# Kernel optimization log

Measured on AMD Instinct MI355X. Metric: run time of the kernel, lower is better.

The kernel has to match this reference:

```python
import jax, jax.numpy as jnp
import numpy as np

B, R, C, H, W = 8, 4, 64, 128, 128
RF, E = 256, 8
C2 = 2 * C
K = 3


def setup_inputs() -> dict:
    key = jax.random.key(0)
    ks = jax.random.split(key, 8)
    return {
        "x": jax.random.normal(ks[0], (B, C, H, W), jnp.float32),
        "routing": jax.random.normal(ks[1], (B, R, RF), jnp.float32),
        # nn.Linear(routing_features, num_experts)
        "routing_W": jax.random.normal(ks[2], (RF, E), jnp.float32) * 0.05,
        "routing_b": jnp.zeros((E,), jnp.float32),
        # CondConv2d expert weights: (E, Cout, Cin, k, k)
        "W1": jax.random.normal(ks[3], (E, C2, C, K, K), jnp.float32) * 0.04,
        "prelu_a": jnp.float32(0.25),  # PReLU single shared parameter
        "W2": jax.random.normal(ks[4], (E, C, C2, K, K), jnp.float32) * 0.03,
        # self-routing Linear(2*in_features, num_experts)
        "sr_W": jax.random.normal(ks[5], (C2, E), jnp.float32) * 0.08,
        "sr_b": jnp.zeros((E,), jnp.float32),
        # conv_output: Conv2d(in_features, 1, kernel_size=1) with bias
        "Wout": jax.random.normal(ks[6], (1, C), jnp.float32) * 0.1,
        "bout": jnp.zeros((1,), jnp.float32),
    }


def _prelu(x, a):
    return jnp.where(x >= 0, x, a * x)


def _cond_conv(x, rw, Wexp):
    # x: (B,Cin,H,W); rw: (B,E); Wexp: (E,Cout,Cin,k,k)
    # per-sample mixed kernel, then per-sample conv (vmap over batch)
    w = jnp.einsum('be,eoikl->boikl', rw, Wexp)
    def one(xi, wi):
        return jax.lax.conv_general_dilated(
            xi[None], wi, window_strides=(1, 1), padding=[(1, 1), (1, 1)])[0]
    return jax.vmap(one)(x, w)


def reference(x, routing, routing_W, routing_b, W1, prelu_a, W2, sr_W, sr_b, Wout, bout):
    rw = jax.nn.sigmoid(routing @ routing_W + routing_b)  # (B,R,E)
    rw = jnp.transpose(rw, (1, 0, 2))                     # (R,B,E)

    def per_head(rw_r):
        xc = _prelu(_cond_conv(x, rw_r, W1), prelu_a)      # (B,C2,H,W)
        pooled = xc.mean(axis=(2, 3))                      # adaptive_avg_pool2d(.,1)
        srw = pooled @ sr_W + sr_b                         # no sigmoid (per source)
        xc2 = _prelu(_cond_conv(xc, srw, W2), prelu_a)     # (B,C,H,W)
        out = jnp.einsum('bchw,oc->bohw', xc2, Wout)       # 1x1 conv
        return out + bout[None, :, None, None]             # (B,1,H,W)

    res = jax.vmap(per_head)(rw)                           # (R,B,1,H,W)
    return jnp.transpose(res[:, :, 0], (1, 0, 2, 3))       # (B,R,H,W)
```

## Files before the change

### kernel.cpp

```cpp
#include <hip/hip_runtime.h>
#include <stdint.h>


typedef _Float16 f16_t;
typedef _Float16 f16x8 __attribute__((ext_vector_type(8)));
typedef _Float16 f16x4 __attribute__((ext_vector_type(4)));
typedef float    f32x4 __attribute__((ext_vector_type(4)));

#define B_   8
#define R_   4
#define C_   64
#define C2_  128
#define H_   128
#define W_   128
#define E_   8
#define RF_  256
#define WP_  130
#define HP_  130

__device__ __forceinline__ f32x4 mfma16(f16x8 a, f16x8 b, f32x4 c) {
  return __builtin_amdgcn_mfma_f32_16x16x32_f16(a, b, c, 0, 0, 0);
}

__device__ __forceinline__ void gl16(const f16_t* g, f16_t* l) {
  __builtin_amdgcn_global_load_lds(
      (const __attribute__((address_space(1))) unsigned int*)(const void*)g,
      (__attribute__((address_space(3))) unsigned int*)(void*)l, 16, 0, 0);
}

__device__ __host__ __forceinline__ int sig(int n) { return (n ^ (n >> 2)) & 3; }

__global__ void k_rw(const float* __restrict__ routing, const float* __restrict__ rW,
                     const float* __restrict__ rB, float* __restrict__ rw,
                     float* __restrict__ pooled4) {
  int t = threadIdx.x;
  #pragma unroll
  for (int i = 0; i < 16; ++i) pooled4[i*256 + t] = 0.f;
  int e = t & 7, b = (t >> 3) & 7, r = t >> 6;
  float acc = rB[e];
  for (int f = 0; f < RF_; ++f)
    acc += routing[(b*R_ + r)*RF_ + f] * rW[f*E_ + e];
  rw[(r*B_ + b)*E_ + e] = 1.0f / (1.0f + __expf(-acc));
}

__global__ void k_zero(f16_t* __restrict__ xbt, f16_t* __restrict__ xct,
                       size_t xct_stride) {
  const f16x8 z = {0,0,0,0,0,0,0,0};
  int t = blockIdx.x*256 + threadIdx.x;
  if (t < 16640) {
    int ch = t & 7, u = t >> 3;
    int pix = u % 130; u /= 130;
    int rs = u & 1, b = u >> 1;
    *(f16x8*)&xbt[((size_t)(b*HP_ + rs*129)*WP_ + pix)*C_ + ch*8] = z;
    return;
  }
  t -= 16640;
  if (t < 133120) {
    int ch = t & 15, u = t >> 4;
    int pix = u % 130; u /= 130;
    int rs = u & 1; u >>= 1;
    int b = u & 7, r = u >> 3;
    *(f16x8*)&xct[(size_t)r*xct_stride + ((size_t)(b*HP_ + rs*129)*WP_ + pix)*C2_ + ch*8] = z;
    return;
  }
  t -= 133120;
  if (t < 131072) {
    int ch = t & 15, u = t >> 4;
    int hp = (u & 127) + 1; u >>= 7;
    int cs = u & 1; u >>= 1;
    int b = u & 7, r = u >> 3;
    *(f16x8*)&xct[(size_t)r*xct_stride + ((size_t)(b*HP_ + hp)*WP_ + cs*129)*C2_ + ch*8] = z;
  }
}

__global__ void k_xt(const float* __restrict__ x, f16_t* __restrict__ xbt) {
  int wh = blockIdx.x, h = blockIdx.y, b = blockIdx.z;
  int t = threadIdx.x;
  int w0 = wh * 64;
  __shared__ float tile[64][65];
  #pragma unroll
  for (int rep = 0; rep < 16; ++rep) {
    int idx = rep*256 + t;
    int c = idx >> 6, w = idx & 63;
    tile[c][w] = x[((size_t)(b*C_ + c)*H_ + h)*W_ + w0 + w];
  }
  __syncthreads();
  #pragma unroll
  for (int rep = 0; rep < 16; ++rep) {
    int idx = rep*256 + t;
    int w = idx >> 6, c = idx & 63;
    xbt[((size_t)(b*HP_ + h + 1)*WP_ + (w0 + w + 1))*C_ + c] = (f16_t)tile[c][w];
  }
  if (t < 64) {
    if (wh == 0) xbt[((size_t)(b*HP_ + h + 1)*WP_ + 0)*C_ + t]   = (f16_t)0.0f;
    else         xbt[((size_t)(b*HP_ + h + 1)*WP_ + 129)*C_ + t] = (f16_t)0.0f;
  }
}

__global__ void k_mix1(const float* __restrict__ rw, const float* __restrict__ W1,
                       f16_t* __restrict__ w1m) {
  int gid = blockIdx.x*256 + threadIdx.x;
  int cq4 = gid & 15;
  int s   = (gid >> 4) % 9;
  int t2  = (gid >> 4) / 9;
  int co  = t2 & 127;
  int rb  = t2 >> 7;
  float o0=0.f,o1=0.f,o2=0.f,o3=0.f;
  #pragma unroll
  for (int e = 0; e < E_; ++e) {
    float rv = rw[rb*E_ + e];
    const float* wp = W1 + (size_t)((e*C2_ + co)*C_ + cq4*4)*9 + s;
    o0 += rv*wp[0]; o1 += rv*wp[9]; o2 += rv*wp[18]; o3 += rv*wp[27];
  }
  f16x4 pk; pk[0]=(f16_t)o0; pk[1]=(f16_t)o1; pk[2]=(f16_t)o2; pk[3]=(f16_t)o3;
  int cb  = cq4 >> 3;
  int q   = (cq4 >> 1) & 3;
  int off = (cq4 & 1) * 4;
  size_t row = ((size_t)(rb*2 + cb)*128 + co);
  *(f16x4*)&w1m[row*288 + (size_t)(s*4 + (q ^ sig(co)))*8 + off] = pk;
}

__global__ void k_mix2(const float* __restrict__ pooled, const float* __restrict__ srW,
                       const float* __restrict__ srb, const float* __restrict__ W2,
                       f16_t* __restrict__ w2m, size_t w2m_stride, int r0) {
  const int r = r0 + blockIdx.y;
  const float* pooled_r = pooled + (size_t)r*B_*C2_;
  f16_t* w2m_r = w2m + (size_t)r*w2m_stride;
  __shared__ float sw[64];
  int t = threadIdx.x;
  if (t < 64) {
    int b = t >> 3, e = t & 7;
    float acc = srb[e];
    for (int c = 0; c < C2_; ++c)
      acc += pooled_r[b*C2_ + c] * (1.0f/16384.0f) * srW[c*E_ + e];
    sw[t] = acc;
  }
  __syncthreads();
  int gid = blockIdx.x*256 + t;
  int c2q = gid & 31;
  int s   = (gid >> 5) % 9;
  int t2  = (gid >> 5) / 9;
  int co  = t2 & 63;
  int b   = t2 >> 6;
  float o0=0.f,o1=0.f,o2=0.f,o3=0.f;
  #pragma unroll
  for (int e = 0; e < E_; ++e) {
    float rv = sw[b*E_ + e];
    const float* wp = W2 + (size_t)((e*C_ + co)*C2_ + c2q*4)*9 + s;
    o0 += rv*wp[0]; o1 += rv*wp[9]; o2 += rv*wp[18]; o3 += rv*wp[27];
  }
  f16x4 pk; pk[0]=(f16_t)o0; pk[1]=(f16_t)o1; pk[2]=(f16_t)o2; pk[3]=(f16_t)o3;
  int it  = c2q >> 3;
  int q   = (c2q >> 1) & 3;
  int off = (c2q & 1) * 4;
  size_t row = ((size_t)b*4 + it)*64 + co;
  *(f16x4*)&w2m_r[row*288 + (size_t)(s*4 + (q ^ sig(co)))*8 + off] = pk;
}

__global__ __launch_bounds__(512, 2) void k_conv1(
    const f16_t* __restrict__ xbt, const f16_t* __restrict__ w1m,
    const float* __restrict__ pa, f16_t* __restrict__ xct, size_t xct_stride,
    float* __restrict__ pooled, int r0)
{
  const int bx = blockIdx.x;
  const int b = bx & 7, h0 = (bx >> 3) << 2;
  const int r = r0 + blockIdx.z;
  f16_t* xct_r = xct + (size_t)blockIdx.z*xct_stride;
  float* pooled_r = pooled + (size_t)r*B_*C2_;
  const int tid = threadIdx.x;
  const int lane = tid & 63;
  const int wid = tid >> 6;
  const int wrow = wid >> 1, wm = wid & 1;
  const int l15 = lane & 15, l4 = lane >> 4;
  __shared__ __align__(16) f16_t lA[128*288];
  __shared__ __align__(16) f16_t lB[3120*8];

  const int xorA = (l4 ^ sig(l15)) << 4;
  int xorB[3];
  #pragma unroll
  for (int dw = 0; dw < 3; ++dw) xorB[dw] = (l4 ^ sig(l15 + dw)) << 4;

  f32x4 acc[4][8];
  #pragma unroll
  for (int i=0;i<4;++i)
    #pragma unroll
    for (int j=0;j<8;++j) acc[i][j] = (f32x4){0.f,0.f,0.f,0.f};

  const int rb = r*B_ + b;
  const f16_t* w1base = w1m + (size_t)rb*2*128*288;
  const f16_t* xb = xbt + ((size_t)(b*HP_ + h0))*WP_*C_;

  for (int cb = 0; cb < 2; ++cb) {
    __syncthreads();
    #pragma unroll
    for (int k = 0; k < 9; ++k) {
      int u = k*512 + tid;
      gl16(w1base + (size_t)cb*128*288 + (size_t)u*8, &lA[u*8]);
    }
    #pragma unroll
    for (int k = 0; k < 6; ++k) {
      int u = k*512 + tid;
      int lr = u / 520, rem = u - lr*520;
      int pix = rem >> 2, cq = (rem & 3) ^ sig(pix);
      gl16(xb + ((size_t)lr*WP_ + pix)*C_ + cb*32 + cq*8, &lB[u*8]);
    }
    if (tid < 48) {
      int u = 3072 + tid;
      int rem = u - 2600;
      int pix = rem >> 2, cq = (rem & 3) ^ sig(pix);
      gl16(xb + ((size_t)5*WP_ + pix)*C_ + cb*32 + cq*8, &lB[u*8]);
    }
    __syncthreads();
    __builtin_amdgcn_s_setprio(1);
    #pragma unroll
    for (int s = 0; s < 9; ++s) {
      const int dh = s / 3, dw = s % 3;
      f16x8 af[4];
      #pragma unroll
      for (int fm = 0; fm < 4; ++fm)
        af[fm] = *(const f16x8*)((const char*)lA
                   + (wm*64 + fm*16 + l15)*576 + s*64 + xorA);
      const char* bbase = (const char*)lB + (wrow + dh)*8320 + (l15 + dw)*64 + xorB[dw];
      f16x8 bf[8];
      #pragma unroll
      for (int fn = 0; fn < 8; ++fn)
        bf[fn] = *(const f16x8*)(bbase + fn*1024);
      #pragma unroll
      for (int fm = 0; fm < 4; ++fm)
        #pragma unroll
        for (int fn = 0; fn < 8; ++fn)
          acc[fm][fn] = mfma16(af[fm], bf[fn], acc[fm][fn]);
    }
    __builtin_amdgcn_s_setprio(0);
  }

  const float a = pa[0];
  float ps[4][4];
  #pragma unroll
  for (int fm=0;fm<4;++fm)
    #pragma unroll
    for (int j=0;j<4;++j) ps[fm][j] = 0.f;
  #pragma unroll
  for (int fm = 0; fm < 4; ++fm)
    #pragma unroll
    for (int fn = 0; fn < 8; ++fn)
      #pragma unroll
      for (int j = 0; j < 4; ++j) {
        float v = acc[fm][fn][j];
        v = (v >= 0.f) ? v : a*v;
        acc[fm][fn][j] = v;
        ps[fm][j] += v;
      }
  #pragma unroll
  for (int fm = 0; fm < 4; ++fm)
    #pragma unroll
    for (int j = 0; j < 4; ++j) {
      float s = ps[fm][j];
      s += __shfl_xor(s, 1, 64);
      s += __shfl_xor(s, 2, 64);
      s += __shfl_xor(s, 4, 64);
      s += __shfl_xor(s, 8, 64);
      if (l15 == 0)
        atomicAdd(&pooled_r[b*C2_ + wm*64 + fm*16 + l4*4 + j], s);
    }
  #pragma unroll
  for (int t4 = 0; t4 < 4; ++t4) {
    __syncthreads();
    if (wrow == t4) {
      #pragma unroll
      for (int fm = 0; fm < 4; ++fm)
        #pragma unroll
        for (int fn = 0; fn < 8; ++fn) {
          f16x4 pk;
          #pragma unroll
          for (int j = 0; j < 4; ++j) pk[j] = (f16_t)acc[fm][fn][j];
          int pix = fn*16 + l15;
          *(f16x4*)((char*)lB + pix*336 + wm*160 + (fm*16 + l4*4)*2) = pk;
        }
    }
    __syncthreads();
    #pragma unroll
    for (int k = 0; k < 4; ++k) {
      int idx = tid + 512*k;
      int pix = idx >> 4, u = idx & 15;
      f16x8 v = *(const f16x8*)((const char*)lB + pix*336 + u*16 + ((u >= 8) ? 32 : 0));
      *(f16x8*)(xct_r + ((size_t)(b*HP_ + h0 + t4 + 1)*WP_ + pix + 1)*C2_ + u*8) = v;
    }
  }
}

__global__ __launch_bounds__(512, 2) void k_conv2(
    const f16_t* __restrict__ xct, size_t xct_stride,
    const f16_t* __restrict__ w2m, size_t w2m_stride,
    const float* __restrict__ pa, const float* __restrict__ Wout,
    const float* __restrict__ bout, float* __restrict__ out, int r0)
{
  const int bx = blockIdx.x;
  const int b = bx & 7, h0 = (bx >> 3) << 3;
  const int r = r0 + blockIdx.y;
  const int tid = threadIdx.x;
  const int lane = tid & 63;
  const int wid = tid >> 6;
  const int l15 = lane & 15, l4 = lane >> 4;
  __shared__ __align__(16) f16_t lA[64*288];
  __shared__ __align__(16) f16_t lB[5200*8];

  const int xorA = (l4 ^ sig(l15)) << 4;
  int xorB[3];
  #pragma unroll
  for (int dw = 0; dw < 3; ++dw) xorB[dw] = (l4 ^ sig(l15 + dw)) << 4;

  f32x4 acc[4][8];
  #pragma unroll
  for (int i=0;i<4;++i)
    #pragma unroll
    for (int j=0;j<8;++j) acc[i][j] = (f32x4){0.f,0.f,0.f,0.f};

  const f16_t* w2base = w2m + (size_t)r*w2m_stride + (size_t)b*4*64*288;
  const f16_t* xb = xct + (size_t)blockIdx.y*xct_stride + ((size_t)(b*HP_ + h0))*WP_*C2_;

  for (int it = 0; it < 4; ++it) {
    __syncthreads();
    #pragma unroll
    for (int k = 0; k < 4; ++k) {
      int u = k*512 + tid;
      gl16(w2base + (size_t)it*64*288 + (size_t)u*8, &lA[u*8]);
    }
    if (tid < 256) {
      int u = 2048 + tid;
      gl16(w2base + (size_t)it*64*288 + (size_t)u*8, &lA[u*8]);
    }
    #pragma unroll
    for (int k = 0; k < 10; ++k) {
      int u = k*512 + tid;
      int lr = u / 520, rem = u - lr*520;
      int pix = rem >> 2, cq = (rem & 3) ^ sig(pix);
      gl16(xb + ((size_t)lr*WP_ + pix)*C2_ + it*32 + cq*8, &lB[u*8]);
    }
    if (tid < 80) {
      int u = 5120 + tid;
      int rem = u - 4680;
      int pix = rem >> 2, cq = (rem & 3) ^ sig(pix);
      gl16(xb + ((size_t)9*WP_ + pix)*C2_ + it*32 + cq*8, &lB[u*8]);
    }
    __syncthreads();
    __builtin_amdgcn_s_setprio(1);
    #pragma unroll
    for (int s = 0; s < 9; ++s) {
      const int dh = s / 3, dw = s % 3;
      f16x8 af[4];
      #pragma unroll
      for (int fm = 0; fm < 4; ++fm)
        af[fm] = *(const f16x8*)((const char*)lA + (fm*16 + l15)*576 + s*64 + xorA);
      const char* bbase = (const char*)lB + (wid + dh)*8320 + (l15 + dw)*64 + xorB[dw];
      f16x8 bf[8];
      #pragma unroll
      for (int fn = 0; fn < 8; ++fn)
        bf[fn] = *(const f16x8*)(bbase + fn*1024);
      #pragma unroll
      for (int fm = 0; fm < 4; ++fm)
        #pragma unroll
        for (int fn = 0; fn < 8; ++fn)
          acc[fm][fn] = mfma16(af[fm], bf[fn], acc[fm][fn]);
    }
    __builtin_amdgcn_s_setprio(0);
  }

  const float a  = pa[0];
  const float bo = bout[0];
  float wr_[4][4];
  #pragma unroll
  for (int fm = 0; fm < 4; ++fm)
    #pragma unroll
    for (int j = 0; j < 4; ++j)
      wr_[fm][j] = Wout[fm*16 + l4*4 + j];
  float* orow = out + ((size_t)((b*R_ + r)*H_ + h0 + wid))*W_;
  #pragma unroll
  for (int fn = 0; fn < 8; ++fn) {
    float s = 0.f;
    #pragma unroll
    for (int fm = 0; fm < 4; ++fm)
      #pragma unroll
      for (int j = 0; j < 4; ++j) {
        float v = acc[fm][fn][j];
        v = (v >= 0.f) ? v : a*v;
        s += wr_[fm][j]*v;
      }
    s += __shfl_xor(s, 16, 64);
    s += __shfl_xor(s, 32, 64);
    if (lane < 16)
      orow[fn*16 + lane] = s + bo;
  }
}

extern "C" void kernel_launch(void* const* d_in, const int* in_sizes, int n_in,
                              void* d_out, int out_size, void* d_ws, size_t ws_size,
                              hipStream_t stream) {
  (void)in_sizes; (void)n_in; (void)out_size;
  const float* x       = (const float*)d_in[0];
  const float* routing = (const float*)d_in[1];
  const float* rW      = (const float*)d_in[2];
  const float* rB      = (const float*)d_in[3];
  const float* W1      = (const float*)d_in[4];
  const float* pa      = (const float*)d_in[5];
  const float* W2      = (const float*)d_in[6];
  const float* srW     = (const float*)d_in[7];
  const float* srb     = (const float*)d_in[8];
  const float* Wout    = (const float*)d_in[9];
  const float* bout    = (const float*)d_in[10];
  float* out = (float*)d_out;

  const size_t xct_one = (size_t)B_*HP_*WP_*C2_;
  const size_t w2m_one = (size_t)2048*288;
  const size_t need_fused = 17305600ull + 4718592ull + 4*xct_one*2 + 4*w2m_one*2 + 32768ull;
  const bool fused = (ws_size >= need_fused);
  const int ncopies = fused ? 4 : 1;
  const size_t xs = fused ? xct_one : 0;
  const size_t ws2 = fused ? w2m_one : 0;

  char* ws = (char*)d_ws;
  size_t off = 0;
  f16_t* xbt = (f16_t*)(ws + off); off += (size_t)B_*HP_*WP_*C_*2;
  f16_t* w1m = (f16_t*)(ws + off); off += (size_t)8192*288*2;
  f16_t* xct = (f16_t*)(ws + off); off += xct_one*2*ncopies;
  f16_t* w2m = (f16_t*)(ws + off); off += w2m_one*2*ncopies;
  float* rw     = (float*)(ws + off); off += (size_t)R_*B_*E_*4;
  float* pooled = (float*)(ws + off); off += (size_t)R_*B_*C2_*4;

  k_rw  <<<1, 256, 0, stream>>>(routing, rW, rB, rw, pooled);
  k_zero<<<1097, 256, 0, stream>>>(xbt, xct, xs);
  k_xt  <<<dim3(2, H_, B_), 256, 0, stream>>>(x, xbt);
  k_mix1<<<2304, 256, 0, stream>>>(rw, W1, w1m);
  if (fused) {
    k_conv1<<<dim3(256, 1, 4), 512, 0, stream>>>(xbt, w1m, pa, xct, xs, pooled, 0);
    k_mix2 <<<dim3(576, 4), 256, 0, stream>>>(pooled, srW, srb, W2, w2m, ws2, 0);
    k_conv2<<<dim3(128, 4), 512, 0, stream>>>(xct, xs, w2m, ws2, pa, Wout, bout, out, 0);
  } else {
    for (int r = 0; r < R_; ++r) {
      k_conv1<<<dim3(256, 1, 1), 512, 0, stream>>>(xbt, w1m, pa, xct, xs, pooled, r);
      k_mix2 <<<dim3(576, 1), 256, 0, stream>>>(pooled, srW, srb, W2, w2m, ws2, r);
      k_conv2<<<dim3(128, 1), 512, 0, stream>>>(xct, xs, w2m, ws2, pa, Wout, bout, out, r);
    }
  }
}
```

Before: 271.6 us.

## Retile both convs into 3-row, 3-wave blocks and split conv1 output channels

```diff
diff --git a/kernel.cpp b/kernel.cpp
--- a/kernel.cpp
+++ b/kernel.cpp
@@ -113,11 +113,12 @@
     o0 += rv*wp[0]; o1 += rv*wp[9]; o2 += rv*wp[18]; o3 += rv*wp[27];
   }
   f16x4 pk; pk[0]=(f16_t)o0; pk[1]=(f16_t)o1; pk[2]=(f16_t)o2; pk[3]=(f16_t)o3;
+  int coh = co >> 6, co6 = co & 63;
   int cb  = cq4 >> 3;
-  int q   = (cq4 >> 1) & 3;
+  int cqu = (cq4 >> 1) & 3;
   int off = (cq4 & 1) * 4;
-  size_t row = ((size_t)(rb*2 + cb)*128 + co);
-  *(f16x4*)&w1m[row*288 + (size_t)(s*4 + (q ^ sig(co)))*8 + off] = pk;
+  size_t row = ((size_t)(rb*2 + coh)*2 + cb)*64 + co6;
+  *(f16x4*)&w1m[row*288 + (size_t)(s*4 + (cqu ^ sig(co6)))*8 + off] = pk;
 }
 
 __global__ void k_mix2(const float* __restrict__ pooled, const float* __restrict__ srW,
@@ -151,29 +152,31 @@
   }
   f16x4 pk; pk[0]=(f16_t)o0; pk[1]=(f16_t)o1; pk[2]=(f16_t)o2; pk[3]=(f16_t)o3;
   int it  = c2q >> 3;
-  int q   = (c2q >> 1) & 3;
+  int cqu = (c2q >> 1) & 3;
   int off = (c2q & 1) * 4;
   size_t row = ((size_t)b*4 + it)*64 + co;
-  *(f16x4*)&w2m_r[row*288 + (size_t)(s*4 + (q ^ sig(co)))*8 + off] = pk;
-}
-
-__global__ __launch_bounds__(512, 2) void k_conv1(
+  *(f16x4*)&w2m_r[row*288 + (size_t)(s*4 + (cqu ^ sig(co)))*8 + off] = pk;
+}
+
+__global__ __launch_bounds__(192, 2) void k_conv1(
     const f16_t* __restrict__ xbt, const f16_t* __restrict__ w1m,
     const float* __restrict__ pa, f16_t* __restrict__ xct, size_t xct_stride,
     float* __restrict__ pooled, int r0)
 {
   const int bx = blockIdx.x;
-  const int b = bx & 7, h0 = (bx >> 3) << 2;
+  const int b = bx & 7;
+  const int bh = bx >> 3;
+  const int h0 = (bh < 42) ? 3*bh : 125;
+  const int coh = blockIdx.y;
   const int r = r0 + blockIdx.z;
   f16_t* xct_r = xct + (size_t)blockIdx.z*xct_stride;
   float* pooled_r = pooled + (size_t)r*B_*C2_;
   const int tid = threadIdx.x;
   const int lane = tid & 63;
   const int wid = tid >> 6;
-  const int wrow = wid >> 1, wm = wid & 1;
   const int l15 = lane & 15, l4 = lane >> 4;
-  __shared__ __align__(16) f16_t lA[128*288];
-  __shared__ __align__(16) f16_t lB[3120*8];
+  __shared__ __align__(16) f16_t lA[64*288];
+  __shared__ __align__(16) f16_t lB[2600*8];
 
   const int xorA = (l4 ^ sig(l15)) << 4;
   int xorB[3];
@@ -187,28 +190,28 @@
     for (int j=0;j<8;++j) acc[i][j] = (f32x4){0.f,0.f,0.f,0.f};
 
   const int rb = r*B_ + b;
-  const f16_t* w1base = w1m + (size_t)rb*2*128*288;
+  const f16_t* w1base = w1m + ((size_t)(rb*2 + coh)*2)*64*288;
   const f16_t* xb = xbt + ((size_t)(b*HP_ + h0))*WP_*C_;
 
   for (int cb = 0; cb < 2; ++cb) {
     __syncthreads();
     #pragma unroll
-    for (int k = 0; k < 9; ++k) {
-      int u = k*512 + tid;
-      gl16(w1base + (size_t)cb*128*288 + (size_t)u*8, &lA[u*8]);
-    }
-    #pragma unroll
-    for (int k = 0; k < 6; ++k) {
-      int u = k*512 + tid;
+    for (int k = 0; k < 12; ++k) {
+      int u = k*192 + tid;
+      gl16(w1base + (size_t)cb*64*288 + (size_t)u*8, &lA[u*8]);
+    }
+    #pragma unroll
+    for (int k = 0; k < 13; ++k) {
+      int u = k*192 + tid;
       int lr = u / 520, rem = u - lr*520;
       int pix = rem >> 2, cq = (rem & 3) ^ sig(pix);
       gl16(xb + ((size_t)lr*WP_ + pix)*C_ + cb*32 + cq*8, &lB[u*8]);
     }
-    if (tid < 48) {
-      int u = 3072 + tid;
-      int rem = u - 2600;
+    if (tid < 104) {
+      int u = 2496 + tid;
+      int lr = u / 520, rem = u - lr*520;
       int pix = rem >> 2, cq = (rem & 3) ^ sig(pix);
-      gl16(xb + ((size_t)5*WP_ + pix)*C_ + cb*32 + cq*8, &lB[u*8]);
+      gl16(xb + ((size_t)lr*WP_ + pix)*C_ + cb*32 + cq*8, &lB[u*8]);
     }
     __syncthreads();
     __builtin_amdgcn_s_setprio(1);
@@ -218,13 +221,12 @@
       f16x8 af[4];
       #pragma unroll
       for (int fm = 0; fm < 4; ++fm)
-        af[fm] = *(const f16x8*)((const char*)lA
-                   + (wm*64 + fm*16 + l15)*576 + s*64 + xorA);
-      const char* bbase = (const char*)lB + (wrow + dh)*8320 + (l15 + dw)*64 + xorB[dw];
+        af[fm] = *(const f16x8*)((const char*)lA + (fm*16 + l15)*576 + s*64 + xorA);
+      const char* bb = (const char*)lB + (wid + dh)*8320 + (l15 + dw)*64 + xorB[dw];
       f16x8 bf[8];
       #pragma unroll
       for (int fn = 0; fn < 8; ++fn)
-        bf[fn] = *(const f16x8*)(bbase + fn*1024);
+        bf[fn] = *(const f16x8*)(bb + fn*1024);
       #pragma unroll
       for (int fm = 0; fm < 4; ++fm)
         #pragma unroll
@@ -251,6 +253,7 @@
         acc[fm][fn][j] = v;
         ps[fm][j] += v;
       }
+  const bool skipPool = (h0 == 125) && (wid == 0);
   #pragma unroll
   for (int fm = 0; fm < 4; ++fm)
     #pragma unroll
@@ -260,13 +263,13 @@
       s += __shfl_xor(s, 2, 64);
       s += __shfl_xor(s, 4, 64);
       s += __shfl_xor(s, 8, 64);
-      if (l15 == 0)
-        atomicAdd(&pooled_r[b*C2_ + wm*64 + fm*16 + l4*4 + j], s);
-    }
-  #pragma unroll
-  for (int t4 = 0; t4 < 4; ++t4) {
-    __syncthreads();
-    if (wrow == t4) {
+      if (l15 == 0 && !skipPool)
+        atomicAdd(&pooled_r[b*C2_ + coh*64 + fm*16 + l4*4 + j], s);
+    }
+  #pragma unroll
+  for (int t4 = 0; t4 < 3; ++t4) {
+    __syncthreads();
+    if (wid == t4) {
       #pragma unroll
       for (int fm = 0; fm < 4; ++fm)
         #pragma unroll
@@ -275,35 +278,39 @@
           #pragma unroll
           for (int j = 0; j < 4; ++j) pk[j] = (f16_t)acc[fm][fn][j];
           int pix = fn*16 + l15;
-          *(f16x4*)((char*)lB + pix*336 + wm*160 + (fm*16 + l4*4)*2) = pk;
+          *(f16x4*)((char*)lB + pix*144 + (fm*16 + l4*4)*2) = pk;
         }
     }
     __syncthreads();
     #pragma unroll
-    for (int k = 0; k < 4; ++k) {
-      int idx = tid + 512*k;
-      int pix = idx >> 4, u = idx & 15;
-      f16x8 v = *(const f16x8*)((const char*)lB + pix*336 + u*16 + ((u >= 8) ? 32 : 0));
-      *(f16x8*)(xct_r + ((size_t)(b*HP_ + h0 + t4 + 1)*WP_ + pix + 1)*C2_ + u*8) = v;
-    }
-  }
-}
-
-__global__ __launch_bounds__(512, 2) void k_conv2(
+    for (int k = 0; k < 6; ++k) {
+      int u = k*192 + tid;
+      if (u < 1024) {
+        int pix = u >> 3, q = u & 7;
+        f16x8 v = *(const f16x8*)((const char*)lB + pix*144 + q*16);
+        *(f16x8*)(xct_r + ((size_t)(b*HP_ + h0 + t4 + 1)*WP_ + pix + 1)*C2_ + coh*64 + q*8) = v;
+      }
+    }
+  }
+}
+
+__global__ __launch_bounds__(192, 2) void k_conv2(
     const f16_t* __restrict__ xct, size_t xct_stride,
     const f16_t* __restrict__ w2m, size_t w2m_stride,
     const float* __restrict__ pa, const float* __restrict__ Wout,
     const float* __restrict__ bout, float* __restrict__ out, int r0)
 {
   const int bx = blockIdx.x;
-  const int b = bx & 7, h0 = (bx >> 3) << 3;
+  const int b = bx & 7;
+  const int bh = bx >> 3;
+  const int h0 = (bh < 42) ? 3*bh : 125;
   const int r = r0 + blockIdx.y;
   const int tid = threadIdx.x;
   const int lane = tid & 63;
   const int wid = tid >> 6;
   const int l15 = lane & 15, l4 = lane >> 4;
   __shared__ __align__(16) f16_t lA[64*288];
-  __shared__ __align__(16) f16_t lB[5200*8];
+  __shared__ __align__(16) f16_t lB[2600*8];
 
   const int xorA = (l4 ^ sig(l15)) << 4;
   int xorB[3];
@@ -322,26 +329,22 @@
   for (int it = 0; it < 4; ++it) {
     __syncthreads();
     #pragma unroll
-    for (int k = 0; k < 4; ++k) {
-      int u = k*512 + tid;
+    for (int k = 0; k < 12; ++k) {
+      int u = k*192 + tid;
       gl16(w2base + (size_t)it*64*288 + (size_t)u*8, &lA[u*8]);
     }
-    if (tid < 256) {
-      int u = 2048 + tid;
-      gl16(w2base + (size_t)it*64*288 + (size_t)u*8, &lA[u*8]);
-    }
-    #pragma unroll
-    for (int k = 0; k < 10; ++k) {
-      int u = k*512 + tid;
+    #pragma unroll
+    for (int k = 0; k < 13; ++k) {
+      int u = k*192 + tid;
       int lr = u / 520, rem = u - lr*520;
       int pix = rem >> 2, cq = (rem & 3) ^ sig(pix);
       gl16(xb + ((size_t)lr*WP_ + pix)*C2_ + it*32 + cq*8, &lB[u*8]);
     }
-    if (tid < 80) {
-      int u = 5120 + tid;
-      int rem = u - 4680;
+    if (tid < 104) {
+      int u = 2496 + tid;
+      int lr = u / 520, rem = u - lr*520;
       int pix = rem >> 2, cq = (rem & 3) ^ sig(pix);
-      gl16(xb + ((size_t)9*WP_ + pix)*C2_ + it*32 + cq*8, &lB[u*8]);
+      gl16(xb + ((size_t)lr*WP_ + pix)*C2_ + it*32 + cq*8, &lB[u*8]);
     }
     __syncthreads();
     __builtin_amdgcn_s_setprio(1);
@@ -352,11 +355,11 @@
       #pragma unroll
       for (int fm = 0; fm < 4; ++fm)
         af[fm] = *(const f16x8*)((const char*)lA + (fm*16 + l15)*576 + s*64 + xorA);
-      const char* bbase = (const char*)lB + (wid + dh)*8320 + (l15 + dw)*64 + xorB[dw];
+      const char* bb = (const char*)lB + (wid + dh)*8320 + (l15 + dw)*64 + xorB[dw];
       f16x8 bf[8];
       #pragma unroll
       for (int fn = 0; fn < 8; ++fn)
-        bf[fn] = *(const f16x8*)(bbase + fn*1024);
+        bf[fn] = *(const f16x8*)(bb + fn*1024);
       #pragma unroll
       for (int fm = 0; fm < 4; ++fm)
         #pragma unroll
@@ -432,14 +435,14 @@
   k_xt  <<<dim3(2, H_, B_), 256, 0, stream>>>(x, xbt);
   k_mix1<<<2304, 256, 0, stream>>>(rw, W1, w1m);
   if (fused) {
-    k_conv1<<<dim3(256, 1, 4), 512, 0, stream>>>(xbt, w1m, pa, xct, xs, pooled, 0);
+    k_conv1<<<dim3(344, 2, 4), 192, 0, stream>>>(xbt, w1m, pa, xct, xs, pooled, 0);
     k_mix2 <<<dim3(576, 4), 256, 0, stream>>>(pooled, srW, srb, W2, w2m, ws2, 0);
-    k_conv2<<<dim3(128, 4), 512, 0, stream>>>(xct, xs, w2m, ws2, pa, Wout, bout, out, 0);
+    k_conv2<<<dim3(344, 4), 192, 0, stream>>>(xct, xs, w2m, ws2, pa, Wout, bout, out, 0);
   } else {
     for (int r = 0; r < R_; ++r) {
-      k_conv1<<<dim3(256, 1, 1), 512, 0, stream>>>(xbt, w1m, pa, xct, xs, pooled, r);
+      k_conv1<<<dim3(344, 2, 1), 192, 0, stream>>>(xbt, w1m, pa, xct, xs, pooled, r);
       k_mix2 <<<dim3(576, 1), 256, 0, stream>>>(pooled, srW, srb, W2, w2m, ws2, r);
-      k_conv2<<<dim3(128, 1), 512, 0, stream>>>(xct, xs, w2m, ws2, pa, Wout, bout, out, r);
-    }
-  }
-}
+      k_conv2<<<dim3(344, 1), 192, 0, stream>>>(xct, xs, w2m, ws2, pa, Wout, bout, out, r);
+    }
+  }
+}
```

After: 379.9 us. 39.9% more time.

## Double-buffer weight tiles per kernel row and relayout mixed weights for streaming

Applied to the files above, without the earlier changes.

```diff
diff --git a/kernel.cpp b/kernel.cpp
--- a/kernel.cpp
+++ b/kernel.cpp
@@ -29,6 +29,7 @@
 }
 
 __device__ __host__ __forceinline__ int sig(int n) { return (n ^ (n >> 2)) & 3; }
+__device__ __host__ __forceinline__ int perm(int q) { return ((q & 1) << 4) | ((q >> 1) << 3); }
 
 __global__ void k_rw(const float* __restrict__ routing, const float* __restrict__ rW,
                      const float* __restrict__ rB, float* __restrict__ rw,
@@ -113,11 +114,11 @@
     o0 += rv*wp[0]; o1 += rv*wp[9]; o2 += rv*wp[18]; o3 += rv*wp[27];
   }
   f16x4 pk; pk[0]=(f16_t)o0; pk[1]=(f16_t)o1; pk[2]=(f16_t)o2; pk[3]=(f16_t)o3;
-  int cb  = cq4 >> 3;
-  int q   = (cq4 >> 1) & 3;
-  int off = (cq4 & 1) * 4;
-  size_t row = ((size_t)(rb*2 + cb)*128 + co);
-  *(f16x4*)&w1m[row*288 + (size_t)(s*4 + (q ^ sig(co)))*8 + off] = pk;
+  int cb   = cq4 >> 3;
+  int q    = (cq4 >> 1) & 3;
+  int half = cq4 & 1;
+  size_t unit = (size_t)rb*9216 + (size_t)(cb*9 + s)*512 + q*128 + (co ^ perm(q));
+  *(f16x4*)&w1m[unit*8 + half*4] = pk;
 }
 
 __global__ void k_mix2(const float* __restrict__ pooled, const float* __restrict__ srW,
@@ -150,14 +151,14 @@
     o0 += rv*wp[0]; o1 += rv*wp[9]; o2 += rv*wp[18]; o3 += rv*wp[27];
   }
   f16x4 pk; pk[0]=(f16_t)o0; pk[1]=(f16_t)o1; pk[2]=(f16_t)o2; pk[3]=(f16_t)o3;
-  int it  = c2q >> 3;
-  int q   = (c2q >> 1) & 3;
-  int off = (c2q & 1) * 4;
-  size_t row = ((size_t)b*4 + it)*64 + co;
-  *(f16x4*)&w2m_r[row*288 + (size_t)(s*4 + (q ^ sig(co)))*8 + off] = pk;
-}
-
-__global__ __launch_bounds__(512, 2) void k_conv1(
+  int it   = c2q >> 3;
+  int q    = (c2q >> 1) & 3;
+  int half = c2q & 1;
+  size_t unit = (size_t)b*9216 + (size_t)(it*9 + s)*256 + q*64 + (co ^ perm(q));
+  *(f16x4*)&w2m_r[unit*8 + half*4] = pk;
+}
+
+__global__ __launch_bounds__(512, 1) void k_conv1(
     const f16_t* __restrict__ xbt, const f16_t* __restrict__ w1m,
     const float* __restrict__ pa, f16_t* __restrict__ xct, size_t xct_stride,
     float* __restrict__ pooled, int r0)
@@ -172,13 +173,17 @@
   const int wid = tid >> 6;
   const int wrow = wid >> 1, wm = wid & 1;
   const int l15 = lane & 15, l4 = lane >> 4;
-  __shared__ __align__(16) f16_t lA[128*288];
-  __shared__ __align__(16) f16_t lB[3120*8];
-
-  const int xorA = (l4 ^ sig(l15)) << 4;
-  int xorB[3];
-  #pragma unroll
-  for (int dw = 0; dw < 3; ++dw) xorB[dw] = (l4 ^ sig(l15 + dw)) << 4;
+  __shared__ __align__(16) f16_t lA[2][1536*8];
+  __shared__ __align__(16) f16_t lB[2][3120*8];
+
+  int aoff[4];
+  #pragma unroll
+  for (int fm = 0; fm < 4; ++fm)
+    aoff[fm] = l4*2048 + (((wm*64 + fm*16 + l15) ^ perm(l4)) << 4);
+  int boff[3];
+  #pragma unroll
+  for (int dw = 0; dw < 3; ++dw)
+    boff[dw] = (((l15 + dw)*4 + (l4 ^ sig(l15 + dw))) << 4);
 
   f32x4 acc[4][8];
   #pragma unroll
@@ -186,52 +191,64 @@
     #pragma unroll
     for (int j=0;j<8;++j) acc[i][j] = (f32x4){0.f,0.f,0.f,0.f};
 
-  const int rb = r*B_ + b;
-  const f16_t* w1base = w1m + (size_t)rb*2*128*288;
+  const f16_t* w1base = w1m + (size_t)(r*B_ + b)*9216*8;
   const f16_t* xb = xbt + ((size_t)(b*HP_ + h0))*WP_*C_;
 
+  #define STAGE_A1(buf, ph) {                                              \
+    int base_ = ((ph)/3)*4608 + ((ph)%3)*1536;                             \
+    _Pragma("unroll")                                                      \
+    for (int k_ = 0; k_ < 3; ++k_) {                                       \
+      int u_ = k_*512 + tid;                                               \
+      gl16(w1base + (size_t)(base_ + u_)*8, &lA[buf][u_*8]);               \
+    } }
+  #define STAGE_B1(buf, cb) {                                              \
+    _Pragma("unroll")                                                      \
+    for (int k_ = 0; k_ < 6; ++k_) {                                       \
+      int u_ = k_*512 + tid;                                               \
+      int lr_ = u_/520, rem_ = u_ - lr_*520;                               \
+      int pix_ = rem_ >> 2, cq_ = (rem_ & 3) ^ sig(pix_);                  \
+      gl16(xb + ((size_t)lr_*WP_ + pix_)*C_ + (cb)*32 + cq_*8, &lB[buf][u_*8]); \
+    }                                                                      \
+    if (tid < 48) {                                                        \
+      int u_ = 3072 + tid;                                                 \
+      int rem_ = u_ - 2600;                                                \
+      int pix_ = rem_ >> 2, cq_ = (rem_ & 3) ^ sig(pix_);                  \
+      gl16(xb + ((size_t)5*WP_ + pix_)*C_ + (cb)*32 + cq_*8, &lB[buf][u_*8]); \
+    } }
+
+  STAGE_B1(0, 0);
+  STAGE_A1(0, 0);
+  __syncthreads();
+
+  int ab = 0;
   for (int cb = 0; cb < 2; ++cb) {
-    __syncthreads();
-    #pragma unroll
-    for (int k = 0; k < 9; ++k) {
-      int u = k*512 + tid;
-      gl16(w1base + (size_t)cb*128*288 + (size_t)u*8, &lA[u*8]);
-    }
-    #pragma unroll
-    for (int k = 0; k < 6; ++k) {
-      int u = k*512 + tid;
-      int lr = u / 520, rem = u - lr*520;
-      int pix = rem >> 2, cq = (rem & 3) ^ sig(pix);
-      gl16(xb + ((size_t)lr*WP_ + pix)*C_ + cb*32 + cq*8, &lB[u*8]);
-    }
-    if (tid < 48) {
-      int u = 3072 + tid;
-      int rem = u - 2600;
-      int pix = rem >> 2, cq = (rem & 3) ^ sig(pix);
-      gl16(xb + ((size_t)5*WP_ + pix)*C_ + cb*32 + cq*8, &lB[u*8]);
-    }
-    __syncthreads();
-    __builtin_amdgcn_s_setprio(1);
-    #pragma unroll
-    for (int s = 0; s < 9; ++s) {
-      const int dh = s / 3, dw = s % 3;
-      f16x8 af[4];
+    for (int dh = 0; dh < 3; ++dh) {
+      const int p = cb*3 + dh;
+      if (p == 0) { STAGE_B1(1, 1); }
+      if (p < 5)  { STAGE_A1(ab^1, p+1); }
+      const char* Ab = (const char*)lA[ab];
+      const char* Bb = (const char*)lB[cb];
+      __builtin_amdgcn_s_setprio(1);
       #pragma unroll
-      for (int fm = 0; fm < 4; ++fm)
-        af[fm] = *(const f16x8*)((const char*)lA
-                   + (wm*64 + fm*16 + l15)*576 + s*64 + xorA);
-      const char* bbase = (const char*)lB + (wrow + dh)*8320 + (l15 + dw)*64 + xorB[dw];
-      f16x8 bf[8];
-      #pragma unroll
-      for (int fn = 0; fn < 8; ++fn)
-        bf[fn] = *(const f16x8*)(bbase + fn*1024);
-      #pragma unroll
-      for (int fm = 0; fm < 4; ++fm)
+      for (int dw = 0; dw < 3; ++dw) {
+        f16x8 af[4], bf[8];
+        #pragma unroll
+        for (int fm = 0; fm < 4; ++fm)
+          af[fm] = *(const f16x8*)(Ab + dw*8192 + aoff[fm]);
+        const char* bb = Bb + (wrow + dh)*8320 + boff[dw];
         #pragma unroll
         for (int fn = 0; fn < 8; ++fn)
-          acc[fm][fn] = mfma16(af[fm], bf[fn], acc[fm][fn]);
-    }
-    __builtin_amdgcn_s_setprio(0);
+          bf[fn] = *(const f16x8*)(bb + fn*1024);
+        #pragma unroll
+        for (int fm = 0; fm < 4; ++fm)
+          #pragma unroll
+          for (int fn = 0; fn < 8; ++fn)
+            acc[fm][fn] = mfma16(af[fm], bf[fn], acc[fm][fn]);
+      }
+      __builtin_amdgcn_s_setprio(0);
+      __syncthreads();
+      ab ^= 1;
+    }
   }
 
   const float a = pa[0];
@@ -263,6 +280,7 @@
       if (l15 == 0)
         atomicAdd(&pooled_r[b*C2_ + wm*64 + fm*16 + l4*4 + j], s);
     }
+  char* lso = (char*)&lB[0][0];
   #pragma unroll
   for (int t4 = 0; t4 < 4; ++t4) {
     __syncthreads();
@@ -275,7 +293,7 @@
           #pragma unroll
           for (int j = 0; j < 4; ++j) pk[j] = (f16_t)acc[fm][fn][j];
           int pix = fn*16 + l15;
-          *(f16x4*)((char*)lB + pix*336 + wm*160 + (fm*16 + l4*4)*2) = pk;
+          *(f16x4*)(lso + pix*336 + wm*160 + (fm*16 + l4*4)*2) = pk;
         }
     }
     __syncthreads();
@@ -283,13 +301,15 @@
     for (int k = 0; k < 4; ++k) {
       int idx = tid + 512*k;
       int pix = idx >> 4, u = idx & 15;
-      f16x8 v = *(const f16x8*)((const char*)lB + pix*336 + u*16 + ((u >= 8) ? 32 : 0));
+      f16x8 v = *(const f16x8*)(lso + pix*336 + u*16 + ((u >= 8) ? 32 : 0));
       *(f16x8*)(xct_r + ((size_t)(b*HP_ + h0 + t4 + 1)*WP_ + pix + 1)*C2_ + u*8) = v;
     }
   }
-}
-
-__global__ __launch_bounds__(512, 2) void k_conv2(
+  #undef STAGE_A1
+  #undef STAGE_B1
+}
+
+__global__ __launch_bounds__(512, 1) void k_conv2(
     const f16_t* __restrict__ xct, size_t xct_stride,
     const f16_t* __restrict__ w2m, size_t w2m_stride,
     const float* __restrict__ pa, const float* __restrict__ Wout,
@@ -302,13 +322,17 @@
   const int lane = tid & 63;
   const int wid = tid >> 6;
   const int l15 = lane & 15, l4 = lane >> 4;
-  __shared__ __align__(16) f16_t lA[64*288];
+  __shared__ __align__(16) f16_t lA[2][768*8];
   __shared__ __align__(16) f16_t lB[5200*8];
 
-  const int xorA = (l4 ^ sig(l15)) << 4;
-  int xorB[3];
-  #pragma unroll
-  for (int dw = 0; dw < 3; ++dw) xorB[dw] = (l4 ^ sig(l15 + dw)) << 4;
+  int aoff[4];
+  #pragma unroll
+  for (int fm = 0; fm < 4; ++fm)
+    aoff[fm] = l4*1024 + (((fm*16 + l15) ^ perm(l4)) << 4);
+  int boff[3];
+  #pragma unroll
+  for (int dw = 0; dw < 3; ++dw)
+    boff[dw] = (((l15 + dw)*4 + (l4 ^ sig(l15 + dw))) << 4);
 
   f32x4 acc[4][8];
   #pragma unroll
@@ -316,54 +340,60 @@
     #pragma unroll
     for (int j=0;j<8;++j) acc[i][j] = (f32x4){0.f,0.f,0.f,0.f};
 
-  const f16_t* w2base = w2m + (size_t)r*w2m_stride + (size_t)b*4*64*288;
+  const f16_t* w2base = w2m + (size_t)r*w2m_stride + (size_t)b*9216*8;
   const f16_t* xb = xct + (size_t)blockIdx.y*xct_stride + ((size_t)(b*HP_ + h0))*WP_*C2_;
 
+  #define STAGE_A2(buf, ph) {                                              \
+    int base_ = ((ph)/3)*2304 + ((ph)%3)*768;                              \
+    { int u_ = tid;                                                        \
+      gl16(w2base + (size_t)(base_ + u_)*8, &lA[buf][u_*8]); }             \
+    if (tid < 256) { int u_ = 512 + tid;                                   \
+      gl16(w2base + (size_t)(base_ + u_)*8, &lA[buf][u_*8]); } }
+  #define STAGE_B2(it) {                                                   \
+    _Pragma("unroll")                                                      \
+    for (int k_ = 0; k_ < 10; ++k_) {                                      \
+      int u_ = k_*512 + tid;                                               \
+      int lr_ = u_/520, rem_ = u_ - lr_*520;                               \
+      int pix_ = rem_ >> 2, cq_ = (rem_ & 3) ^ sig(pix_);                  \
+      gl16(xb + ((size_t)lr_*WP_ + pix_)*C2_ + (it)*32 + cq_*8, &lB[u_*8]); \
+    }                                                                      \
+    if (tid < 80) {                                                        \
+      int u_ = 5120 + tid;                                                 \
+      int rem_ = u_ - 4680;                                                \
+      int pix_ = rem_ >> 2, cq_ = (rem_ & 3) ^ sig(pix_);                  \
+      gl16(xb + ((size_t)9*WP_ + pix_)*C2_ + (it)*32 + cq_*8, &lB[u_*8]);  \
+    } }
+
+  STAGE_A2(0, 0);
+  int ab = 0;
   for (int it = 0; it < 4; ++it) {
+    STAGE_B2(it);
     __syncthreads();
-    #pragma unroll
-    for (int k = 0; k < 4; ++k) {
-      int u = k*512 + tid;
-      gl16(w2base + (size_t)it*64*288 + (size_t)u*8, &lA[u*8]);
-    }
-    if (tid < 256) {
-      int u = 2048 + tid;
-      gl16(w2base + (size_t)it*64*288 + (size_t)u*8, &lA[u*8]);
-    }
-    #pragma unroll
-    for (int k = 0; k < 10; ++k) {
-      int u = k*512 + tid;
-      int lr = u / 520, rem = u - lr*520;
-      int pix = rem >> 2, cq = (rem & 3) ^ sig(pix);
-      gl16(xb + ((size_t)lr*WP_ + pix)*C2_ + it*32 + cq*8, &lB[u*8]);
-    }
-    if (tid < 80) {
-      int u = 5120 + tid;
-      int rem = u - 4680;
-      int pix = rem >> 2, cq = (rem & 3) ^ sig(pix);
-      gl16(xb + ((size_t)9*WP_ + pix)*C2_ + it*32 + cq*8, &lB[u*8]);
-    }
-    __syncthreads();
-    __builtin_amdgcn_s_setprio(1);
-    #pragma unroll
-    for (int s = 0; s < 9; ++s) {
-      const int dh = s / 3, dw = s % 3;
-      f16x8 af[4];
+    for (int dh = 0; dh < 3; ++dh) {
+      const int p = it*3 + dh;
+      if (p < 11) { STAGE_A2(ab^1, p+1); }
+      const char* Ab = (const char*)lA[ab];
+      __builtin_amdgcn_s_setprio(1);
       #pragma unroll
-      for (int fm = 0; fm < 4; ++fm)
-        af[fm] = *(const f16x8*)((const char*)lA + (fm*16 + l15)*576 + s*64 + xorA);
-      const char* bbase = (const char*)lB + (wid + dh)*8320 + (l15 + dw)*64 + xorB[dw];
-      f16x8 bf[8];
-      #pragma unroll
-      for (int fn = 0; fn < 8; ++fn)
-        bf[fn] = *(const f16x8*)(bbase + fn*1024);
-      #pragma unroll
-      for (int fm = 0; fm < 4; ++fm)
+      for (int dw = 0; dw < 3; ++dw) {
+        f16x8 af[4], bf[8];
+        #pragma unroll
+        for (int fm = 0; fm < 4; ++fm)
+          af[fm] = *(const f16x8*)(Ab + dw*4096 + aoff[fm]);
+        const char* bb = (const char*)lB + (wid + dh)*8320 + boff[dw];
         #pragma unroll
         for (int fn = 0; fn < 8; ++fn)
-          acc[fm][fn] = mfma16(af[fm], bf[fn], acc[fm][fn]);
-    }
-    __builtin_amdgcn_s_setprio(0);
+          bf[fn] = *(const f16x8*)(bb + fn*1024);
+        #pragma unroll
+        for (int fm = 0; fm < 4; ++fm)
+          #pragma unroll
+          for (int fn = 0; fn < 8; ++fn)
+            acc[fm][fn] = mfma16(af[fm], bf[fn], acc[fm][fn]);
+      }
+      __builtin_amdgcn_s_setprio(0);
+      __syncthreads();
+      ab ^= 1;
+    }
   }
 
   const float a  = pa[0];
@@ -391,6 +421,8 @@
     if (lane < 16)
       orow[fn*16 + lane] = s + bo;
   }
+  #undef STAGE_A2
+  #undef STAGE_B2
 }
 
 extern "C" void kernel_launch(void* const* d_in, const int* in_sizes, int n_in,
@@ -411,7 +443,7 @@
   float* out = (float*)d_out;
 
   const size_t xct_one = (size_t)B_*HP_*WP_*C2_;
-  const size_t w2m_one = (size_t)2048*288;
+  const size_t w2m_one = (size_t)8*9216*8;
   const size_t need_fused = 17305600ull + 4718592ull + 4*xct_one*2 + 4*w2m_one*2 + 32768ull;
   const bool fused = (ws_size >= need_fused);
   const int ncopies = fused ? 4 : 1;
@@ -421,7 +453,7 @@
   char* ws = (char*)d_ws;
   size_t off = 0;
   f16_t* xbt = (f16_t*)(ws + off); off += (size_t)B_*HP_*WP_*C_*2;
-  f16_t* w1m = (f16_t*)(ws + off); off += (size_t)8192*288*2;
+  f16_t* w1m = (f16_t*)(ws + off); off += (size_t)32*9216*16;
   f16_t* xct = (f16_t*)(ws + off); off += xct_one*2*ncopies;
   f16_t* w2m = (f16_t*)(ws + off); off += w2m_one*2*ncopies;
   float* rw     = (float*)(ws + off); off += (size_t)R_*B_*E_*4;
```

Measured after the change: 336.6 us (median of 2 runs). 23.9% more time.
